# Kernel optimization log

Measured on AMD Instinct MI355X. Metric: run time of the kernel, lower is better.

## Reference

```python
import jax, jax.numpy as jnp
import numpy as np

DECODING_TIME = 1.0
EPS = 1e-6


def setup_inputs() -> dict:
    key = jax.random.key(0)
    k1, k2, k3 = jax.random.split(key, 3)
    B, C, S = 1024, 100, 1000
    u = jax.random.normal(k1, (B, C), dtype=jnp.float32)
    # SPD covariance: cov = A A^T / C + 0.1 I
    A = jax.random.normal(k2, (B, C, C), dtype=jnp.float32)
    cov = jnp.einsum('bij,bkj->bik', A, A) / C + 0.1 * jnp.eye(C, dtype=jnp.float32)
    sample_point = jax.random.normal(k3, (S, C), dtype=jnp.float32)
    return {"u": u, "cov": cov, "sample_point": sample_point}


def reference(u, cov, sample_point):
    # Faithful translation of functional.gaussian_sampling_pred:
    # scale mean/cov by decoding time, regularize cov with eps*I,
    # batched Cholesky, affine-transform the standard-normal sample
    # points, softmax over classes, average over samples.
    C = u.shape[-1]
    scaled_u = u * DECODING_TIME                              # [B, C]
    scaled_cov = cov * DECODING_TIME + EPS * jnp.eye(C, dtype=cov.dtype)
    L = jnp.linalg.cholesky(scaled_cov)                       # [B, C, C]
    # samples = u + z @ L^T, z = sample_point  -> [B, S, C]
    samples = scaled_u[:, None, :] + jnp.einsum('sc,bdc->bsd', sample_point, L)
    probs = jax.nn.softmax(samples, axis=-1)                  # [B, S, C]
    pred = jnp.mean(probs, axis=1)                            # [B, C] (normalise=True)
    return pred
```

## Files before the change

kernel.cpp:

```cpp
#include <hip/hip_runtime.h>


#define CC   100
#define SS   1000
#define EPSF 1e-6f
#define NB   16
#define NDT  7
#define NCS  4
#define NST  63

typedef short  s8 __attribute__((ext_vector_type(8)));
typedef float  f4 __attribute__((ext_vector_type(4)));

__device__ inline unsigned short f2bf(float x) {
    unsigned u = __float_as_uint(x);
    return (unsigned short)((u + 0x7fffu + ((u >> 16) & 1u)) >> 16);
}

__global__ __launch_bounds__(256)
void zconv_kernel(const float* __restrict__ z, unsigned short* __restrict__ zb) {
    const int stile = blockIdx.x;
    const int cs = threadIdx.x >> 6;
    const int l  = threadIdx.x & 63;
    const int s  = stile * 16 + (l & 15);
    const int c0 = cs * 32 + (l >> 4) * 8;
    unsigned short v[8];
    #pragma unroll
    for (int j = 0; j < 8; ++j) {
        const int c = c0 + j;
        const float x = (s < SS && c < CC) ? z[(size_t)s * CC + c] : 0.0f;
        v[j] = f2bf(x);
    }
    uint4 pk;
    pk.x = (unsigned)v[0] | ((unsigned)v[1] << 16);
    pk.y = (unsigned)v[2] | ((unsigned)v[3] << 16);
    pk.z = (unsigned)v[4] | ((unsigned)v[5] << 16);
    pk.w = (unsigned)v[6] | ((unsigned)v[7] << 16);
    reinterpret_cast<uint4*>(zb)[(stile * NCS + cs) * 64 + l] = pk;
}

template<int NPAN>
__device__ inline void panel_factor(float* __restrict__ M, int jb, int l) {
    float P0r[NPAN], P1r[NPAN];
    const int i1 = l + 64;
    #pragma unroll
    for (int jj = 0; jj < NPAN; ++jj) {
        P0r[jj] = M[(jb + jj) * CC + l];
        P1r[jj] = (i1 < CC) ? M[(jb + jj) * CC + i1] : 0.0f;
    }
    #pragma unroll
    for (int jj = 0; jj < NPAN; ++jj) {
        const int j = jb + jj;
        const float dsrc  = (j & 64) ? P1r[jj] : P0r[jj];
        const float val   = __shfl(dsrc, j & 63);
        const float dinv  = rsqrtf(val);
        const float s     = val * dinv;
        const float dinv2 = dinv * dinv;
        #pragma unroll
        for (int kk = jj + 1; kk < NPAN; ++kk) {
            const int k = jb + kk;
            const float tsrc = (k & 64) ? P1r[jj] : P0r[jj];
            const float t = __shfl(tsrc, k & 63) * dinv2;
            P0r[kk] -= P0r[jj] * t;
            P1r[kk] -= P1r[jj] * t;
        }
        P0r[jj] = (l == j) ? s : ((l > j) ? P0r[jj] * dinv : P0r[jj]);
        P1r[jj] = (i1 == j) ? s : ((i1 > j) ? P1r[jj] * dinv : P1r[jj]);
    }
    #pragma unroll
    for (int jj = 0; jj < NPAN; ++jj) {
        M[(jb + jj) * CC + l] = P0r[jj];
        if (i1 < CC) M[(jb + jj) * CC + i1] = P1r[jj];
    }
}

__global__ __launch_bounds__(256, 4)
void chol_kernel(const float* __restrict__ cov, unsigned short* __restrict__ Lb) {
    __shared__ float M[CC * CC];
    const int tid = threadIdx.x;
    const int w   = tid >> 6;
    const int l   = tid & 63;
    const int b   = blockIdx.x;

    const float4* c4 = reinterpret_cast<const float4*>(cov + (size_t)b * CC * CC);
    for (int t = tid; t < CC * CC / 4; t += 256)
        reinterpret_cast<float4*>(M)[t] = c4[t];
    __syncthreads();
    for (int d = tid; d < CC; d += 256) M[d * CC + d] += EPSF;
    __syncthreads();

    for (int jb = 0; jb < CC; jb += NB) {
        const int jend = (jb + NB < CC) ? jb + NB : CC;

        if (w == 0) {
            if (jend - jb == NB) panel_factor<NB>(M, jb, l);
            else                 panel_factor<CC - (CC / NB) * NB>(M, jb, l);
        }
        __syncthreads();

        if (jend < CC) {
            const int i0 = jend + l;
            const int i1 = i0 + 64;
            float P0[NB], P1[NB];
            #pragma unroll
            for (int jj = 0; jj < NB; ++jj) {
                P0[jj] = (i0 < CC) ? M[(jb + jj) * CC + i0] : 0.0f;
                P1[jj] = (i1 < CC) ? M[(jb + jj) * CC + i1] : 0.0f;
            }
            #pragma unroll 2
            for (int k = jend + w; k < CC; k += 4) {
                float bk[NB];
                #pragma unroll
                for (int jj = 0; jj < NB; ++jj)
                    bk[jj] = M[(jb + jj) * CC + k];
                if (i0 < CC) {
                    float acc = M[k * CC + i0];
                    #pragma unroll
                    for (int jj = 0; jj < NB; ++jj) acc -= P0[jj] * bk[jj];
                    M[k * CC + i0] = acc;
                }
                if (i1 < CC) {
                    float acc = M[k * CC + i1];
                    #pragma unroll
                    for (int jj = 0; jj < NB; ++jj) acc -= P1[jj] * bk[jj];
                    M[k * CC + i1] = acc;
                }
            }
        }
        __syncthreads();
    }

    const int tx = l & 15;
    const int ty = l >> 4;
    unsigned short* outp = Lb + (size_t)b * (NDT * NCS * 64 * 8);
    for (int f = w; f < NDT * NCS; f += 4) {
        const int dt = f >> 2, cs = f & 3;
        const int d  = dt * 16 + tx;
        const int c0 = cs * 32 + ty * 8;
        unsigned short v[8];
        #pragma unroll
        for (int j = 0; j < 8; ++j) {
            const int c = c0 + j;
            float x = 0.0f;
            if (d < CC && c <= d) x = M[c * CC + d];
            v[j] = f2bf(x);
        }
        uint4 pk;
        pk.x = (unsigned)v[0] | ((unsigned)v[1] << 16);
        pk.y = (unsigned)v[2] | ((unsigned)v[3] << 16);
        pk.z = (unsigned)v[4] | ((unsigned)v[5] << 16);
        pk.w = (unsigned)v[6] | ((unsigned)v[7] << 16);
        reinterpret_cast<uint4*>(outp)[f * 64 + l] = pk;
    }
}

__global__ __launch_bounds__(256, 1)
void pred_kernel(const float* __restrict__ u,
                 const unsigned short* __restrict__ Lb,
                 const unsigned short* __restrict__ zb,
                 float* __restrict__ out) {
    __shared__ float red[4 * NDT * 16];
    const int tid = threadIdx.x, b = blockIdx.x;
    const int w  = tid >> 6;
    const int l  = tid & 63;
    const int li = l & 15;
    const int hi = l >> 4;

    s8 Bf[NDT][NCS];
    const s8* Lb8 = reinterpret_cast<const s8*>(Lb + (size_t)b * (NDT * NCS * 64 * 8));
    #pragma unroll
    for (int dt = 0; dt < NDT; ++dt)
        #pragma unroll
        for (int cs = 0; cs < NCS; ++cs)
            Bf[dt][cs] = Lb8[(dt * NCS + cs) * 64 + l];

    float ureg[NDT];
    #pragma unroll
    for (int dt = 0; dt < NDT; ++dt) {
        const int d = dt * 16 + li;
        ureg[dt] = (d < CC) ? u[(size_t)b * CC + d] : 0.0f;
    }

    float meanAcc[NDT];
    #pragma unroll
    for (int dt = 0; dt < NDT; ++dt) meanAcc[dt] = 0.0f;

    const s8* zb8 = reinterpret_cast<const s8*>(zb);

    for (int st = w; st < NST; st += 4) {
        s8 Af[NCS];
        #pragma unroll
        for (int cs = 0; cs < NCS; ++cs)
            Af[cs] = zb8[(st * NCS + cs) * 64 + l];

        f4 acc[NDT];
        #pragma unroll
        for (int dt = 0; dt < NDT; ++dt) acc[dt] = (f4){0.f, 0.f, 0.f, 0.f};

        #pragma unroll
        for (int cs = 0; cs < NCS; ++cs)
            #pragma unroll
            for (int dt = 0; dt < NDT; ++dt)
                acc[dt] = __builtin_amdgcn_mfma_f32_16x16x32_bf16(
                              Af[cs], Bf[dt][cs], acc[dt], 0, 0, 0);

        #pragma unroll
        for (int r = 0; r < 4; ++r) {
            const int s = st * 16 + hi * 4 + r;
            float tv[NDT];
            #pragma unroll
            for (int dt = 0; dt < NDT; ++dt) {
                float x = acc[dt][r] + ureg[dt];
                if (dt == NDT - 1 && li >= 4) x = -1e30f;
                tv[dt] = x;
            }
            float m = tv[0];
            #pragma unroll
            for (int dt = 1; dt < NDT; ++dt) m = fmaxf(m, tv[dt]);
            m = fmaxf(m, __shfl_xor(m, 1));
            m = fmaxf(m, __shfl_xor(m, 2));
            m = fmaxf(m, __shfl_xor(m, 4));
            m = fmaxf(m, __shfl_xor(m, 8));
            float e[NDT], sum = 0.0f;
            #pragma unroll
            for (int dt = 0; dt < NDT; ++dt) {
                e[dt] = __expf(tv[dt] - m);
                sum += e[dt];
            }
            sum += __shfl_xor(sum, 1);
            sum += __shfl_xor(sum, 2);
            sum += __shfl_xor(sum, 4);
            sum += __shfl_xor(sum, 8);
            const float wt = (s < SS) ? 1.0f / sum : 0.0f;
            #pragma unroll
            for (int dt = 0; dt < NDT; ++dt) meanAcc[dt] += e[dt] * wt;
        }
    }

    #pragma unroll
    for (int dt = 0; dt < NDT; ++dt) {
        float v = meanAcc[dt];
        v += __shfl_xor(v, 16);
        v += __shfl_xor(v, 32);
        meanAcc[dt] = v;
    }
    if (l < 16) {
        #pragma unroll
        for (int dt = 0; dt < NDT; ++dt)
            red[(w * NDT + dt) * 16 + l] = meanAcc[dt];
    }
    __syncthreads();
    if (tid < CC) {
        const int dt = tid >> 4, li2 = tid & 15;
        const float sum = red[(0 * NDT + dt) * 16 + li2]
                        + red[(1 * NDT + dt) * 16 + li2]
                        + red[(2 * NDT + dt) * 16 + li2]
                        + red[(3 * NDT + dt) * 16 + li2];
        out[(size_t)b * CC + tid] = sum * (1.0f / (float)SS);
    }
}

extern "C" void kernel_launch(void* const* d_in, const int* in_sizes, int n_in,
                              void* d_out, int out_size, void* d_ws, size_t ws_size,
                              hipStream_t stream) {
    const float* u   = (const float*)d_in[0];
    const float* cov = (const float*)d_in[1];
    const float* z   = (const float*)d_in[2];
    float* outp = (float*)d_out;
    const int B = in_sizes[0] / CC;

    unsigned short* zb = (unsigned short*)d_ws;
    unsigned short* Lbf = (unsigned short*)((char*)d_ws + (1 << 20));

    zconv_kernel<<<dim3(NST), dim3(256), 0, stream>>>(z, zb);
    chol_kernel <<<dim3(B),   dim3(256), 0, stream>>>(cov, Lbf);
    pred_kernel <<<dim3(B),   dim3(256), 0, stream>>>(u, Lbf, zb, outp);
}
```

Measured before the change: 139.8 us.

## Fold mean and log2e into MFMA operands and drop softmax max subtraction

The mean vector u is folded into the GEMM as two extra contraction columns: a bf16 high part and a bf16 residual, multiplied by ones added to z. The padded classes get -1e30 in the same way, and all of L and u is pre-scaled by log2(e) so the softmax uses raw exp2. The MFMA operands are swapped so that each lane holds a whole sample row, which replaces the per-row shuffle reductions with a two-step cross-lane sum. The max subtraction is removed and a fast reciprocal is used. Without the max shift, large logits could overflow exp2, so the change relies on the value range of the inputs.

```diff
diff --git a/kernel.cpp b/kernel.cpp
--- a/kernel.cpp
+++ b/kernel.cpp
@@ -1,13 +1,14 @@
 #include <hip/hip_runtime.h>
 
 
-#define CC   100
-#define SS   1000
-#define EPSF 1e-6f
-#define NB   16
-#define NDT  7
-#define NCS  4
-#define NST  63
+#define CC    100
+#define SS    1000
+#define EPSF  1e-6f
+#define NB    16
+#define NDT   7
+#define NCS   4
+#define NST   63
+#define LOG2E 1.44269504088896340736f
 
 typedef short  s8 __attribute__((ext_vector_type(8)));
 typedef float  f4 __attribute__((ext_vector_type(4)));
@@ -15,6 +16,9 @@
 __device__ inline unsigned short f2bf(float x) {
     unsigned u = __float_as_uint(x);
     return (unsigned short)((u + 0x7fffu + ((u >> 16) & 1u)) >> 16);
+}
+__device__ inline float bf2f(unsigned short h) {
+    return __uint_as_float(((unsigned)h) << 16);
 }
 
 __global__ __launch_bounds__(256)
@@ -28,7 +32,9 @@
     #pragma unroll
     for (int j = 0; j < 8; ++j) {
         const int c = c0 + j;
-        const float x = (s < SS && c < CC) ? z[(size_t)s * CC + c] : 0.0f;
+        float x = 0.0f;
+        if (c < CC)      x = (s < SS) ? z[(size_t)s * CC + c] : 0.0f;
+        else if (c <= CC + 1) x = 1.0f;
         v[j] = f2bf(x);
     }
     uint4 pk;
@@ -75,7 +81,8 @@
 }
 
 __global__ __launch_bounds__(256, 4)
-void chol_kernel(const float* __restrict__ cov, unsigned short* __restrict__ Lb) {
+void chol_kernel(const float* __restrict__ cov, const float* __restrict__ u,
+                 unsigned short* __restrict__ Lb) {
     __shared__ float M[CC * CC];
     const int tid = threadIdx.x;
     const int w   = tid >> 6;
@@ -142,7 +149,17 @@
         for (int j = 0; j < 8; ++j) {
             const int c = c0 + j;
             float x = 0.0f;
-            if (d < CC && c <= d) x = M[c * CC + d];
+            if (c < CC) {
+                if (d < CC && c <= d) x = M[c * CC + d] * LOG2E;
+            } else if (c == CC) {
+                if (d < CC) x = bf2f(f2bf(u[(size_t)b * CC + d] * LOG2E));
+                else        x = -1e30f;
+            } else if (c == CC + 1) {
+                if (d < CC) {
+                    const float t = u[(size_t)b * CC + d] * LOG2E;
+                    x = t - bf2f(f2bf(t));
+                }
+            }
             v[j] = f2bf(x);
         }
         uint4 pk;
@@ -155,8 +172,7 @@
 }
 
 __global__ __launch_bounds__(256, 1)
-void pred_kernel(const float* __restrict__ u,
-                 const unsigned short* __restrict__ Lb,
+void pred_kernel(const unsigned short* __restrict__ Lb,
                  const unsigned short* __restrict__ zb,
                  float* __restrict__ out) {
     __shared__ float red[4 * NDT * 16];
@@ -174,16 +190,11 @@
         for (int cs = 0; cs < NCS; ++cs)
             Bf[dt][cs] = Lb8[(dt * NCS + cs) * 64 + l];
 
-    float ureg[NDT];
-    #pragma unroll
-    for (int dt = 0; dt < NDT; ++dt) {
-        const int d = dt * 16 + li;
-        ureg[dt] = (d < CC) ? u[(size_t)b * CC + d] : 0.0f;
-    }
-
-    float meanAcc[NDT];
-    #pragma unroll
-    for (int dt = 0; dt < NDT; ++dt) meanAcc[dt] = 0.0f;
+    float meanAcc[NDT][4];
+    #pragma unroll
+    for (int dt = 0; dt < NDT; ++dt)
+        #pragma unroll
+        for (int r = 0; r < 4; ++r) meanAcc[dt][r] = 0.0f;
 
     const s8* zb8 = reinterpret_cast<const s8*>(zb);
 
@@ -202,60 +213,42 @@
             #pragma unroll
             for (int dt = 0; dt < NDT; ++dt)
                 acc[dt] = __builtin_amdgcn_mfma_f32_16x16x32_bf16(
-                              Af[cs], Bf[dt][cs], acc[dt], 0, 0, 0);
-
+                              Bf[dt][cs], Af[cs], acc[dt], 0, 0, 0);
+
+        float e[NDT][4];
+        float rs = 0.0f;
+        #pragma unroll
+        for (int dt = 0; dt < NDT; ++dt)
+            #pragma unroll
+            for (int r = 0; r < 4; ++r) {
+                const float ev = __builtin_amdgcn_exp2f(acc[dt][r]);
+                e[dt][r] = ev;
+                rs += ev;
+            }
+        rs += __shfl_xor(rs, 16);
+        rs += __shfl_xor(rs, 32);
+        const float wgt = (st * 16 + li < SS) ? __builtin_amdgcn_rcpf(rs) : 0.0f;
+        #pragma unroll
+        for (int dt = 0; dt < NDT; ++dt)
+            #pragma unroll
+            for (int r = 0; r < 4; ++r) meanAcc[dt][r] += e[dt][r] * wgt;
+    }
+
+    #pragma unroll
+    for (int dt = 0; dt < NDT; ++dt)
         #pragma unroll
         for (int r = 0; r < 4; ++r) {
-            const int s = st * 16 + hi * 4 + r;
-            float tv[NDT];
-            #pragma unroll
-            for (int dt = 0; dt < NDT; ++dt) {
-                float x = acc[dt][r] + ureg[dt];
-                if (dt == NDT - 1 && li >= 4) x = -1e30f;
-                tv[dt] = x;
-            }
-            float m = tv[0];
-            #pragma unroll
-            for (int dt = 1; dt < NDT; ++dt) m = fmaxf(m, tv[dt]);
-            m = fmaxf(m, __shfl_xor(m, 1));
-            m = fmaxf(m, __shfl_xor(m, 2));
-            m = fmaxf(m, __shfl_xor(m, 4));
-            m = fmaxf(m, __shfl_xor(m, 8));
-            float e[NDT], sum = 0.0f;
-            #pragma unroll
-            for (int dt = 0; dt < NDT; ++dt) {
-                e[dt] = __expf(tv[dt] - m);
-                sum += e[dt];
-            }
-            sum += __shfl_xor(sum, 1);
-            sum += __shfl_xor(sum, 2);
-            sum += __shfl_xor(sum, 4);
-            sum += __shfl_xor(sum, 8);
-            const float wt = (s < SS) ? 1.0f / sum : 0.0f;
-            #pragma unroll
-            for (int dt = 0; dt < NDT; ++dt) meanAcc[dt] += e[dt] * wt;
-        }
-    }
-
-    #pragma unroll
-    for (int dt = 0; dt < NDT; ++dt) {
-        float v = meanAcc[dt];
-        v += __shfl_xor(v, 16);
-        v += __shfl_xor(v, 32);
-        meanAcc[dt] = v;
-    }
-    if (l < 16) {
-        #pragma unroll
-        for (int dt = 0; dt < NDT; ++dt)
-            red[(w * NDT + dt) * 16 + l] = meanAcc[dt];
-    }
+            float v = meanAcc[dt][r];
+            v += __shfl_xor(v, 1);
+            v += __shfl_xor(v, 2);
+            v += __shfl_xor(v, 4);
+            v += __shfl_xor(v, 8);
+            if (li == 0) red[w * (NDT * 16) + dt * 16 + hi * 4 + r] = v;
+        }
     __syncthreads();
     if (tid < CC) {
-        const int dt = tid >> 4, li2 = tid & 15;
-        const float sum = red[(0 * NDT + dt) * 16 + li2]
-                        + red[(1 * NDT + dt) * 16 + li2]
-                        + red[(2 * NDT + dt) * 16 + li2]
-                        + red[(3 * NDT + dt) * 16 + li2];
+        const float sum = red[tid] + red[NDT * 16 + tid] +
+                          red[2 * NDT * 16 + tid] + red[3 * NDT * 16 + tid];
         out[(size_t)b * CC + tid] = sum * (1.0f / (float)SS);
     }
 }
@@ -273,6 +266,6 @@
     unsigned short* Lbf = (unsigned short*)((char*)d_ws + (1 << 20));
 
     zconv_kernel<<<dim3(NST), dim3(256), 0, stream>>>(z, zb);
-    chol_kernel <<<dim3(B),   dim3(256), 0, stream>>>(cov, Lbf);
-    pred_kernel <<<dim3(B),   dim3(256), 0, stream>>>(u, Lbf, zb, outp);
-}
+    chol_kernel <<<dim3(B),   dim3(256), 0, stream>>>(cov, u, Lbf);
+    pred_kernel <<<dim3(B),   dim3(256), 0, stream>>>(Lbf, zb, outp);
+}
```

Result: faster. 114.7 us (-17.9%).
